# Kernel optimization log

Measured on AMD Instinct MI355X. Metric: run time of the kernel, lower is better.

Reference implementation:

```python
import jax, jax.numpy as jnp
import numpy as np

H = 1024

def _lin(x, W, b):
    # torch Linear: y = x @ W.T + b, W shape (out, in)
    return x @ W.T + b

def setup_inputs() -> dict:
    key = jax.random.key(0)
    ks = jax.random.split(key, 16)
    B, S = 128, 128
    s = 1.0 / np.sqrt(H)
    inp = {
        'facts': jax.random.normal(ks[0], (B, S, H), jnp.float32),
        'questions': jax.random.normal(ks[1], (B, 1, H), jnp.float32),
        'prevM': jax.random.normal(ks[2], (B, 1, H), jnp.float32),
        # AttentionGRUCell params
        'Wr': jax.random.normal(ks[3], (H, H), jnp.float32) * s,
        'br': jnp.zeros((H,), jnp.float32),
        'Ur': jax.random.normal(ks[4], (H, H), jnp.float32) * s,
        'bur': jnp.zeros((H,), jnp.float32),
        'W': jax.random.normal(ks[5], (H, H), jnp.float32) * s,
        'bw': jnp.zeros((H,), jnp.float32),
        'U': jax.random.normal(ks[6], (H, H), jnp.float32) * s,
        'bu': jnp.zeros((H,), jnp.float32),
        # interaction MLP
        'Wz1': jax.random.normal(ks[7], (H, 4 * H), jnp.float32) * (1.0 / np.sqrt(4 * H)),
        'bz1': jnp.zeros((H,), jnp.float32),
        'Wz2': jax.random.normal(ks[8], (1, H), jnp.float32) * s,
        'bz2': jnp.zeros((1,), jnp.float32),
        # next memory
        'Wm': jax.random.normal(ks[9], (H, 3 * H), jnp.float32) * (1.0 / np.sqrt(3 * H)),
        'bm': jnp.zeros((H,), jnp.float32),
    }
    return inp

def _forward(facts, questions, prevM, Wr, br, Ur, bur, W, bw, U, bu, Wz1, bz1, Wz2, bz2, Wm, bm):
    B, S, E = facts.shape
    q = questions  # (B,1,H) broadcasts
    m = prevM
    # gated interaction features: (B,S,4H)
    z = jnp.concatenate([facts * q, facts * m,
                         jnp.abs(facts - q), jnp.abs(facts - m)], axis=2)
    G = _lin(jnp.tanh(_lin(z, Wz1, bz1)), Wz2, bz2)  # (B,S,1)
    G = jax.nn.softmax(G[..., 0], axis=1)            # (B,S)

    # attention GRU scan over sentences
    def step(C, xs):
        fact, g = xs                                  # fact (B,H), g (B,)
        r = jax.nn.sigmoid(_lin(fact, Wr, br) + _lin(C, Ur, bur))
        h_tilda = jnp.tanh(_lin(fact, W, bw) + r * _lin(C, U, bu))
        g = g[:, None]
        C = g * h_tilda + (1.0 - g) * C
        return C, None

    C0 = jnp.zeros((B, E), facts.dtype)
    C, _ = jax.lax.scan(step, C0, (facts.transpose(1, 0, 2), G.T))

    concat = jnp.concatenate([prevM[:, 0], C, questions[:, 0]], axis=1)  # (B,3H)
    next_mem = jax.nn.relu(_lin(concat, Wm, bm))
    return next_mem[:, None, :]  # (B,1,H)

def reference(facts, questions, prevM, Wr, br, Ur, bur, W, bw, U, bu, Wz1, bz1, Wz2, bz2, Wm, bm):
    return _forward(facts, questions, prevM, Wr, br, Ur, bur, W, bw, U, bu, Wz1, bz1, Wz2, bz2, Wm, bm)
```

## Files before the change

### kernel.cpp

```cpp
#include <hip/hip_runtime.h>
#include <hip/hip_bf16.h>

typedef __attribute__((ext_vector_type(8))) short short8;
typedef __attribute__((ext_vector_type(4))) short short4v;
typedef __attribute__((ext_vector_type(4))) float floatx4;
typedef __attribute__((ext_vector_type(4))) unsigned int uint4v;

using bf16 = __hip_bfloat16;

#define DEVI __device__ __forceinline__

static constexpr size_t OFF_SCORE  = 0;
static constexpr size_t OFF_XCC    = 65536;
static constexpr size_t OFF_CPUB   = OFF_XCC + 4096;
static constexpr size_t ZERO_BYTES = OFF_CPUB + 524288;
static constexpr size_t OFF_G      = OFF_CPUB   + 1048576;
static constexpr size_t OFF_BIASR  = OFF_G      + 65536;
static constexpr size_t OFF_CFIN   = OFF_BIASR  + 4096;
static constexpr size_t OFF_CONCAT = OFF_CFIN   + 524288;
static constexpr size_t OFF_FACTS  = OFF_CONCAT + 786432;
static constexpr size_t OFF_WZ1    = OFF_FACTS  + 33554432ull;
static constexpr size_t OFF_WRW    = OFF_WZ1    + 8388608ull;
static constexpr size_t OFF_URU    = OFF_WRW    + 4194304ull;
static constexpr size_t OFF_WM     = OFF_URU    + 4194304ull;
static constexpr size_t OFF_P      = OFF_WM     + 6291456ull;

DEVI float sigm_f(float x){ return 1.f/(1.f + __expf(-x)); }
DEVI float tanh_f(float x){ float e = __expf(2.f*x); return 1.f - 2.f/(e + 1.f); }

DEVI uint4v ld_cg_u128(const uint4v* p){
  uint4v r;
  asm volatile("global_load_dwordx4 %0, %1, off sc0 sc1" : "=v"(r) : "v"(p) : "memory");
  return r;
}
DEVI uint4v ld_l2_u128(const uint4v* p){
  uint4v r;
  asm volatile("global_load_dwordx4 %0, %1, off sc0" : "=v"(r) : "v"(p) : "memory");
  return r;
}
DEVI void st_cg_u64(unsigned long long* p, unsigned long long v){
  asm volatile("global_store_dwordx2 %0, %1, off sc0 sc1" : : "v"(p), "v"(v) : "memory");
}
DEVI void st_l2_u64(unsigned long long* p, unsigned long long v){
  asm volatile("global_store_dwordx2 %0, %1, off" : : "v"(p), "v"(v) : "memory");
}
DEVI void waitcnt_vm0(){ asm volatile("s_waitcnt vmcnt(0)" ::: "memory"); }

__global__ void cast_f32_bf16(const float* __restrict__ src, bf16* __restrict__ dst, int n){
  int i = (blockIdx.x*256 + threadIdx.x)*4;
  if (i >= n) return;
  float4 v = *(const float4*)(src + i);
  union { bf16 h[4]; short4v s; } u;
  u.h[0] = __float2bfloat16(v.x); u.h[1] = __float2bfloat16(v.y);
  u.h[2] = __float2bfloat16(v.z); u.h[3] = __float2bfloat16(v.w);
  *(short4v*)(dst + i) = u.s;
}

__global__ void add_bias_k(const float* __restrict__ a, const float* __restrict__ b, float* __restrict__ o){
  int i = blockIdx.x*256 + threadIdx.x;
  if (i < 1024) o[i] = a[i] + b[i];
}

__global__ void softmax128(const float* __restrict__ score, float* __restrict__ G){
  int b = blockIdx.x, t = threadIdx.x;
  int lane = t & 63, wv = t >> 6;
  float v = score[b*128 + t];
  float mx = v;
  #pragma unroll
  for (int m = 1; m < 64; m <<= 1) mx = fmaxf(mx, __shfl_xor(mx, m));
  __shared__ float r1[2], r2[2];
  if (lane == 0) r1[wv] = mx;
  __syncthreads();
  mx = fmaxf(r1[0], r1[1]);
  float e = __expf(v - mx);
  float sm = e;
  #pragma unroll
  for (int m = 1; m < 64; m <<= 1) sm += __shfl_xor(sm, m);
  if (lane == 0) r2[wv] = sm;
  __syncthreads();
  sm = r2[0] + r2[1];
  G[b*128 + t] = e / sm;
}

__global__ void build_concat(const float* __restrict__ prevM, const float* __restrict__ Cfin,
                             const float* __restrict__ q, bf16* __restrict__ out){
  int i = (blockIdx.x*256 + threadIdx.x)*4;
  if (i >= 128*3072) return;
  int b = i / 3072, k = i % 3072;
  const float* src = (k < 1024) ? (prevM + b*1024 + k)
                   : (k < 2048) ? (Cfin + b*1024 + (k-1024))
                                : (q    + b*1024 + (k-2048));
  float4 v = *(const float4*)src;
  union { bf16 h[4]; short4v s; } u;
  u.h[0] = __float2bfloat16(v.x); u.h[1] = __float2bfloat16(v.y);
  u.h[2] = __float2bfloat16(v.z); u.h[3] = __float2bfloat16(v.w);
  *(short4v*)(out + i) = u.s;
}

__global__ __launch_bounds__(256, 2) void gate_gemm(
    const float* __restrict__ facts, const float* __restrict__ q,
    const float* __restrict__ pm, const bf16* __restrict__ Wz1b,
    const float* __restrict__ bz1, const float* __restrict__ wz2,
    float* __restrict__ score)
{
  constexpr int TS = 80;
  __shared__ bf16 As[128*TS];
  __shared__ bf16 Bs[128*TS];
  __shared__ float qs[1024];
  __shared__ float ms[1024];
  int tid = threadIdx.x;
  int b  = blockIdx.y;
  int n0 = blockIdx.x * 128;
  int w = tid >> 6, lane = tid & 63;
  int wm = w >> 1, wn = w & 1;
  int quad = lane >> 4, col = lane & 15;

  for (int i = tid; i < 1024; i += 256){ qs[i] = q[b*1024 + i]; ms[i] = pm[b*1024 + i]; }
  __syncthreads();

  floatx4 acc[4][4];
  #pragma unroll
  for (int a = 0; a < 4; ++a)
    #pragma unroll
    for (int c = 0; c < 4; ++c) acc[a][c] = (floatx4){0.f,0.f,0.f,0.f};

  for (int it = 0; it < 64; ++it){
    int k0 = it * 64;
    int qd = k0 >> 10;
    int kk0 = k0 & 1023;
    #pragma unroll
    for (int i = 0; i < 4; ++i){
      int c = tid + i*256;
      int r = c >> 3, cc = c & 7;
      int kk = kk0 + cc*8;
      const float* fp = facts + (size_t)(b*128 + r)*1024 + kk;
      float f[8], aux[8];
      *(float4*)(f)   = *(const float4*)(fp);
      *(float4*)(f+4) = *(const float4*)(fp + 4);
      const float* av = (qd == 0 || qd == 2) ? qs : ms;
      *(float4*)(aux)   = *(const float4*)(av + kk);
      *(float4*)(aux+4) = *(const float4*)(av + kk + 4);
      union { bf16 h[8]; short8 s8; } u;
      if (qd < 2){
        #pragma unroll
        for (int j = 0; j < 8; ++j) u.h[j] = __float2bfloat16(f[j]*aux[j]);
      } else {
        #pragma unroll
        for (int j = 0; j < 8; ++j) u.h[j] = __float2bfloat16(fabsf(f[j]-aux[j]));
      }
      *(short8*)&As[r*TS + cc*8] = u.s8;
    }
    #pragma unroll
    for (int i = 0; i < 4; ++i){
      int c = tid + i*256;
      int r = c >> 3, cc = c & 7;
      *(uint4v*)&Bs[r*TS + cc*8] = *(const uint4v*)(Wz1b + (size_t)(n0 + r)*4096 + k0 + cc*8);
    }
    __syncthreads();
    #pragma unroll
    for (int kt = 0; kt < 2; ++kt){
      short8 af[4], bfv[4];
      #pragma unroll
      for (int mt = 0; mt < 4; ++mt)
        af[mt] = *(const short8*)&As[(wm*64 + mt*16 + col)*TS + kt*32 + quad*8];
      #pragma unroll
      for (int nt = 0; nt < 4; ++nt)
        bfv[nt] = *(const short8*)&Bs[(wn*64 + nt*16 + col)*TS + kt*32 + quad*8];
      #pragma unroll
      for (int mt = 0; mt < 4; ++mt)
        #pragma unroll
        for (int nt = 0; nt < 4; ++nt)
          acc[mt][nt] = __builtin_amdgcn_mfma_f32_16x16x32_bf16(af[mt], bfv[nt], acc[mt][nt], 0,0,0);
    }
    __syncthreads();
  }
  #pragma unroll
  for (int mt = 0; mt < 4; ++mt){
    float part[4] = {0.f,0.f,0.f,0.f};
    #pragma unroll
    for (int nt = 0; nt < 4; ++nt){
      int n = n0 + wn*64 + nt*16 + col;
      float b1 = bz1[n], w2 = wz2[n];
      #pragma unroll
      for (int rr = 0; rr < 4; ++rr)
        part[rr] += tanh_f(acc[mt][nt][rr] + b1) * w2;
    }
    #pragma unroll
    for (int rr = 0; rr < 4; ++rr){
      float p = part[rr];
      p += __shfl_xor(p, 1); p += __shfl_xor(p, 2);
      p += __shfl_xor(p, 4); p += __shfl_xor(p, 8);
      if (col == 0)
        atomicAdd(&score[b*128 + wm*64 + mt*16 + quad*4 + rr], p);
    }
  }
}

template<int MODE>
__global__ __launch_bounds__(256, 2) void gemm_bt(
    const bf16* __restrict__ A, const bf16* __restrict__ Bm, int K,
    bf16* __restrict__ Pout, const float* __restrict__ bias, float* __restrict__ out)
{
  constexpr int TS = 80;
  __shared__ bf16 As[128*TS];
  __shared__ bf16 Bs[128*TS];
  int tid = threadIdx.x;
  int m0 = blockIdx.y * 128, n0 = blockIdx.x * 128;
  int w = tid >> 6, lane = tid & 63;
  int wm = w >> 1, wn = w & 1;
  int quad = lane >> 4, col = lane & 15;

  floatx4 acc[4][4];
  #pragma unroll
  for (int a = 0; a < 4; ++a)
    #pragma unroll
    for (int c = 0; c < 4; ++c) acc[a][c] = (floatx4){0.f,0.f,0.f,0.f};

  int nkb = K >> 6;
  for (int it = 0; it < nkb; ++it){
    int k0 = it * 64;
    #pragma unroll
    for (int i = 0; i < 4; ++i){
      int c = tid + i*256;
      int r = c >> 3, cc = c & 7;
      *(uint4v*)&As[r*TS + cc*8] = *(const uint4v*)(A  + (size_t)(m0 + r)*K + k0 + cc*8);
      *(uint4v*)&Bs[r*TS + cc*8] = *(const uint4v*)(Bm + (size_t)(n0 + r)*K + k0 + cc*8);
    }
    __syncthreads();
    #pragma unroll
    for (int kt = 0; kt < 2; ++kt){
      short8 af[4], bfv[4];
      #pragma unroll
      for (int mt = 0; mt < 4; ++mt)
        af[mt] = *(const short8*)&As[(wm*64 + mt*16 + col)*TS + kt*32 + quad*8];
      #pragma unroll
      for (int nt = 0; nt < 4; ++nt)
        bfv[nt] = *(const short8*)&Bs[(wn*64 + nt*16 + col)*TS + kt*32 + quad*8];
      #pragma unroll
      for (int mt = 0; mt < 4; ++mt)
        #pragma unroll
        for (int nt = 0; nt < 4; ++nt)
          acc[mt][nt] = __builtin_amdgcn_mfma_f32_16x16x32_bf16(af[mt], bfv[nt], acc[mt][nt], 0,0,0);
    }
    __syncthreads();
  }
  #pragma unroll
  for (int mt = 0; mt < 4; ++mt)
    #pragma unroll
    for (int nt = 0; nt < 4; ++nt)
      #pragma unroll
      for (int rr = 0; rr < 4; ++rr){
        int m = m0 + wm*64 + mt*16 + quad*4 + rr;
        int n = n0 + wn*64 + nt*16 + col;
        float v = acc[mt][nt][rr];
        if (MODE == 0){
          Pout[((size_t)(m & 127)*128 + (m >> 7))*2048 + n] = __float2bfloat16(v);
        } else {
          out[(size_t)m*1024 + n] = fmaxf(v + bias[n], 0.f);
        }
      }
}

__global__ __launch_bounds__(256, 1) void scan_kernel(
    const bf16* __restrict__ UrU, const bf16* __restrict__ P,
    const float* __restrict__ G, const float* __restrict__ bias_r,
    const float* __restrict__ bw, const float* __restrict__ bu,
    unsigned long long* __restrict__ Cpub, float* __restrict__ Cfinal,
    unsigned int* __restrict__ xcc_slots)
{
  constexpr int CS = 1040;
  __shared__ bf16 Cs[16*CS];
  __shared__ float Qex[2*16*32];
  int tid = threadIdx.x;
  int g  = blockIdx.x & 7;
  int nb = blockIdx.x >> 3;
  int b0 = g * 16, j0 = nb * 32;
  int w = tid >> 6, lane = tid & 63;
  int quad = lane >> 4, col = lane & 15;

  unsigned int my_tag = __builtin_amdgcn_s_getreg(20 | (31u << 11)) + 1u;
  bool fast;
  {
    unsigned int* xs = xcc_slots + g*32;
    if (tid == 0)
      __hip_atomic_store(&xs[nb], my_tag, __ATOMIC_RELAXED, __HIP_MEMORY_SCOPE_AGENT);
    unsigned long long bad;
    for (;;){
      unsigned int v = (lane < 32)
        ? __hip_atomic_load(&xs[lane], __ATOMIC_RELAXED, __HIP_MEMORY_SCOPE_AGENT)
        : my_tag;
      if (__ballot(v == 0u) == 0ull){ bad = __ballot(v != my_tag); break; }
      __builtin_amdgcn_s_sleep(1);
    }
    fast = (bad == 0ull);
  }

  short8 bfrag[32];
  {
    int n = ((w >> 1) << 10) + j0 + ((w & 1) << 4) + col;
    const bf16* src = UrU + (size_t)n*1024 + (quad << 3);
    #pragma unroll
    for (int kt = 0; kt < 32; ++kt) bfrag[kt] = *(const short8*)(src + kt*32);
  }

  int r  = tid >> 4;
  int jp = (tid & 15) * 2;
  float c0 = 0.f, c1 = 0.f;
  float2 brv = *(const float2*)(bias_r + j0 + jp);
  float2 bwv = *(const float2*)(bw     + j0 + jp);
  float2 buv = *(const float2*)(bu     + j0 + jp);

  for (int s = 0; s < 128; ++s){
    const bf16* Ps = P + (size_t)s*(128*2048) + (size_t)(b0 + r)*2048 + j0 + jp;
    unsigned int up1 = *(const unsigned int*)Ps;
    unsigned int up2 = *(const unsigned int*)(Ps + 1024);
    float gg = G[(b0 + r)*128 + s];

    const uint4v* Cg = (const uint4v*)
      (Cpub + (size_t)(s & 1)*65536 + (size_t)b0*512);
    uint4v vv[16];
    unsigned int expct = (unsigned int)s;
    for (;;){
      if (fast){
        #pragma unroll
        for (int i = 0; i < 16; ++i) vv[i] = ld_l2_u128(Cg + tid + i*256);
      } else {
        #pragma unroll
        for (int i = 0; i < 16; ++i) vv[i] = ld_cg_u128(Cg + tid + i*256);
      }
      waitcnt_vm0();
      unsigned int bad = 0;
      #pragma unroll
      for (int i = 0; i < 16; ++i)
        bad |= (vv[i].y ^ expct) | (vv[i].w ^ expct);
      if (__ballot(bad != 0u) == 0ull) break;
      __builtin_amdgcn_s_sleep(1);
    }
    #pragma unroll
    for (int i = 0; i < 16; ++i){
      int p = tid + i*256;
      int rr = p >> 8, pi = p & 255;
      unsigned long long wdat = (unsigned long long)vv[i].x
                              | ((unsigned long long)vv[i].z << 32);
      *(unsigned long long*)&Cs[rr*CS + pi*4] = wdat;
    }
    __syncthreads();

    floatx4 a0 = (floatx4){0.f,0.f,0.f,0.f}, a1 = (floatx4){0.f,0.f,0.f,0.f};
    {
      const bf16* Ap = Cs + col*CS + (quad << 3);
      #pragma unroll
      for (int kt = 0; kt < 16; ++kt){
        short8 a = *(const short8*)(Ap + kt*32);
        a0 = __builtin_amdgcn_mfma_f32_16x16x32_bf16(a, bfrag[kt], a0, 0,0,0);
      }
      #pragma unroll
      for (int kt = 16; kt < 32; ++kt){
        short8 a = *(const short8*)(Ap + kt*32);
        a1 = __builtin_amdgcn_mfma_f32_16x16x32_bf16(a, bfrag[kt], a1, 0,0,0);
      }
    }
    {
      int mi = w >> 1, nh = w & 1;
      #pragma unroll
      for (int rr = 0; rr < 4; ++rr)
        Qex[mi*512 + (quad*4 + rr)*32 + nh*16 + col] = a0[rr] + a1[rr];
    }
    __syncthreads();

    float p1a = __bfloat162float(*(const bf16*)&up1);
    float p1b = __bfloat162float(*((const bf16*)&up1 + 1));
    float p2a = __bfloat162float(*(const bf16*)&up2);
    float p2b = __bfloat162float(*((const bf16*)&up2 + 1));
    float2 q1 = *(const float2*)&Qex[r*32 + jp];
    float2 q2 = *(const float2*)&Qex[512 + r*32 + jp];
    float ra = sigm_f(p1a + q1.x + brv.x);
    float ha = tanh_f(p2a + bwv.x + ra*(q2.x + buv.x));
    c0 = gg*ha + (1.f - gg)*c0;
    float rb = sigm_f(p1b + q1.y + brv.y);
    float hb = tanh_f(p2b + bwv.y + rb*(q2.y + buv.y));
    c1 = gg*hb + (1.f - gg)*c1;

    if (s != 127){
      union { bf16 h[2]; unsigned int u; } pk;
      pk.h[0] = __float2bfloat16(c0);
      pk.h[1] = __float2bfloat16(c1);
      unsigned long long wd = ((unsigned long long)(unsigned int)(s + 1) << 32)
                            | (unsigned long long)pk.u;
      unsigned long long* dst = Cpub + (size_t)((s & 1) ^ 1)*65536
                              + (size_t)(b0 + r)*512 + ((j0 + jp) >> 1);
      if (fast) st_l2_u64(dst, wd); else st_cg_u64(dst, wd);
    }
  }
  *(float2*)&Cfinal[(size_t)(b0 + r)*1024 + j0 + jp] = make_float2(c0, c1);
}

extern "C" void kernel_launch(void* const* d_in, const int* in_sizes, int n_in,
                              void* d_out, int out_size, void* d_ws, size_t ws_size,
                              hipStream_t stream) {
  const float* facts     = (const float*)d_in[0];
  const float* questions = (const float*)d_in[1];
  const float* prevM     = (const float*)d_in[2];
  const float* Wr        = (const float*)d_in[3];
  const float* br        = (const float*)d_in[4];
  const float* Ur        = (const float*)d_in[5];
  const float* bur       = (const float*)d_in[6];
  const float* Wf        = (const float*)d_in[7];
  const float* bw        = (const float*)d_in[8];
  const float* U         = (const float*)d_in[9];
  const float* bu        = (const float*)d_in[10];
  const float* Wz1       = (const float*)d_in[11];
  const float* bz1       = (const float*)d_in[12];
  const float* Wz2       = (const float*)d_in[13];
  const float* Wm        = (const float*)d_in[15];
  const float* bm        = (const float*)d_in[16];
  float* out = (float*)d_out;

  char* ws = (char*)d_ws;
  float*              score   = (float*)(ws + OFF_SCORE);
  unsigned int*       xccs    = (unsigned int*)(ws + OFF_XCC);
  unsigned long long* Cpub    = (unsigned long long*)(ws + OFF_CPUB);
  float*              G       = (float*)(ws + OFF_G);
  float*              bias_r  = (float*)(ws + OFF_BIASR);
  float*              Cfin    = (float*)(ws + OFF_CFIN);
  bf16*               concat  = (bf16*)(ws + OFF_CONCAT);
  bf16*               facts_b = (bf16*)(ws + OFF_FACTS);
  bf16*               Wz1_b   = (bf16*)(ws + OFF_WZ1);
  bf16*               WrW_b   = (bf16*)(ws + OFF_WRW);
  bf16*               UrU_b   = (bf16*)(ws + OFF_URU);
  bf16*               Wm_b    = (bf16*)(ws + OFF_WM);
  bf16*               P       = (bf16*)(ws + OFF_P);

  hipMemsetAsync(ws, 0, ZERO_BYTES, stream);

  cast_f32_bf16<<<16384, 256, 0, stream>>>(facts, facts_b, 16777216);
  cast_f32_bf16<<< 4096, 256, 0, stream>>>(Wz1, Wz1_b, 4194304);
  cast_f32_bf16<<< 1024, 256, 0, stream>>>(Wr, WrW_b,           1048576);
  cast_f32_bf16<<< 1024, 256, 0, stream>>>(Wf, WrW_b + 1048576, 1048576);
  cast_f32_bf16<<< 1024, 256, 0, stream>>>(Ur, UrU_b,           1048576);
  cast_f32_bf16<<< 1024, 256, 0, stream>>>(U,  UrU_b + 1048576, 1048576);
  cast_f32_bf16<<< 3072, 256, 0, stream>>>(Wm, Wm_b, 3145728);
  add_bias_k<<<4, 256, 0, stream>>>(br, bur, bias_r);

  gate_gemm<<<dim3(8, 128), 256, 0, stream>>>(facts, questions, prevM, Wz1_b, bz1, Wz2, score);
  softmax128<<<128, 128, 0, stream>>>(score, G);

  gemm_bt<0><<<dim3(16, 128), 256, 0, stream>>>(facts_b, WrW_b, 1024, P, nullptr, nullptr);

  scan_kernel<<<256, 256, 0, stream>>>(UrU_b, P, G, bias_r, bw, bu, Cpub, Cfin, xccs);

  build_concat<<<384, 256, 0, stream>>>(prevM, Cfin, questions, concat);
  gemm_bt<1><<<dim3(8, 1), 256, 0, stream>>>(concat, Wm_b, 3072, nullptr, bm, out);
}
```

Baseline: 1.031 ms.

## Reuse facts registers across four feature quadrants and prefetch next facts tile

The Wz1 GEMM loop is restructured so each facts chunk is loaded once into registers and reused for all four interaction quadrants (f*q, f*m, |f-q|, |f-m|), instead of reloading facts from global memory per quadrant. The next facts chunk is prefetched into registers while the current one is processed, and B-tile loads are issued into registers before the LDS store. This cuts global facts traffic by about four times and overlaps load latency, at the cost of higher register pressure (two 32-float facts buffers), which could reduce occupancy.

```diff
diff --git a/kernel.cpp b/kernel.cpp
--- a/kernel.cpp
+++ b/kernel.cpp
@@ -124,56 +124,90 @@
     #pragma unroll
     for (int c = 0; c < 4; ++c) acc[a][c] = (floatx4){0.f,0.f,0.f,0.f};
 
-  for (int it = 0; it < 64; ++it){
-    int k0 = it * 64;
-    int qd = k0 >> 10;
-    int kk0 = k0 & 1023;
-    #pragma unroll
-    for (int i = 0; i < 4; ++i){
-      int c = tid + i*256;
-      int r = c >> 3, cc = c & 7;
-      int kk = kk0 + cc*8;
-      const float* fp = facts + (size_t)(b*128 + r)*1024 + kk;
-      float f[8], aux[8];
-      *(float4*)(f)   = *(const float4*)(fp);
-      *(float4*)(f+4) = *(const float4*)(fp + 4);
-      const float* av = (qd == 0 || qd == 2) ? qs : ms;
-      *(float4*)(aux)   = *(const float4*)(av + kk);
-      *(float4*)(aux+4) = *(const float4*)(av + kk + 4);
-      union { bf16 h[8]; short8 s8; } u;
-      if (qd < 2){
-        #pragma unroll
-        for (int j = 0; j < 8; ++j) u.h[j] = __float2bfloat16(f[j]*aux[j]);
-      } else {
-        #pragma unroll
-        for (int j = 0; j < 8; ++j) u.h[j] = __float2bfloat16(fabsf(f[j]-aux[j]));
-      }
-      *(short8*)&As[r*TS + cc*8] = u.s8;
-    }
-    #pragma unroll
-    for (int i = 0; i < 4; ++i){
-      int c = tid + i*256;
-      int r = c >> 3, cc = c & 7;
-      *(uint4v*)&Bs[r*TS + cc*8] = *(const uint4v*)(Wz1b + (size_t)(n0 + r)*4096 + k0 + cc*8);
-    }
-    __syncthreads();
-    #pragma unroll
-    for (int kt = 0; kt < 2; ++kt){
-      short8 af[4], bfv[4];
-      #pragma unroll
-      for (int mt = 0; mt < 4; ++mt)
-        af[mt] = *(const short8*)&As[(wm*64 + mt*16 + col)*TS + kt*32 + quad*8];
-      #pragma unroll
-      for (int nt = 0; nt < 4; ++nt)
-        bfv[nt] = *(const short8*)&Bs[(wn*64 + nt*16 + col)*TS + kt*32 + quad*8];
-      #pragma unroll
-      for (int mt = 0; mt < 4; ++mt)
+  int cc = tid & 7;
+  int r0 = tid >> 3;
+
+  float fc[4][8];
+  float fn[4][8];
+  float q8[8], m8[8];
+
+  #pragma unroll
+  for (int i = 0; i < 4; ++i){
+    const float* fp = facts + (size_t)(b*128 + r0 + i*32)*1024 + cc*8;
+    *(float4*)(fc[i])   = *(const float4*)(fp);
+    *(float4*)(fc[i]+4) = *(const float4*)(fp + 4);
+  }
+
+  for (int it = 0; it < 16; ++it){
+    int kk0 = it * 64;
+    int kk  = kk0 + cc*8;
+    *(float4*)(q8)   = *(const float4*)(qs + kk);
+    *(float4*)(q8+4) = *(const float4*)(qs + kk + 4);
+    *(float4*)(m8)   = *(const float4*)(ms + kk);
+    *(float4*)(m8+4) = *(const float4*)(ms + kk + 4);
+    if (it < 15){
+      #pragma unroll
+      for (int i = 0; i < 4; ++i){
+        const float* fp = facts + (size_t)(b*128 + r0 + i*32)*1024 + kk0 + 64 + cc*8;
+        *(float4*)(fn[i])   = *(const float4*)(fp);
+        *(float4*)(fn[i]+4) = *(const float4*)(fp + 4);
+      }
+    }
+
+    #pragma unroll
+    for (int qd = 0; qd < 4; ++qd){
+      uint4v breg[4];
+      #pragma unroll
+      for (int i = 0; i < 4; ++i)
+        breg[i] = *(const uint4v*)(Wz1b + (size_t)(n0 + r0 + i*32)*4096 + qd*1024 + kk);
+
+      #pragma unroll
+      for (int i = 0; i < 4; ++i){
+        union { bf16 h[8]; short8 s8; } u;
+        if (qd == 0){
+          #pragma unroll
+          for (int j = 0; j < 8; ++j) u.h[j] = __float2bfloat16(fc[i][j]*q8[j]);
+        } else if (qd == 1){
+          #pragma unroll
+          for (int j = 0; j < 8; ++j) u.h[j] = __float2bfloat16(fc[i][j]*m8[j]);
+        } else if (qd == 2){
+          #pragma unroll
+          for (int j = 0; j < 8; ++j) u.h[j] = __float2bfloat16(fabsf(fc[i][j]-q8[j]));
+        } else {
+          #pragma unroll
+          for (int j = 0; j < 8; ++j) u.h[j] = __float2bfloat16(fabsf(fc[i][j]-m8[j]));
+        }
+        *(short8*)&As[(r0 + i*32)*TS + cc*8] = u.s8;
+        *(uint4v*)&Bs[(r0 + i*32)*TS + cc*8] = breg[i];
+      }
+      __syncthreads();
+
+      #pragma unroll
+      for (int kt = 0; kt < 2; ++kt){
+        short8 af[4], bfv[4];
+        #pragma unroll
+        for (int mt = 0; mt < 4; ++mt)
+          af[mt] = *(const short8*)&As[(wm*64 + mt*16 + col)*TS + kt*32 + quad*8];
         #pragma unroll
         for (int nt = 0; nt < 4; ++nt)
-          acc[mt][nt] = __builtin_amdgcn_mfma_f32_16x16x32_bf16(af[mt], bfv[nt], acc[mt][nt], 0,0,0);
-    }
-    __syncthreads();
-  }
+          bfv[nt] = *(const short8*)&Bs[(wn*64 + nt*16 + col)*TS + kt*32 + quad*8];
+        #pragma unroll
+        for (int mt = 0; mt < 4; ++mt)
+          #pragma unroll
+          for (int nt = 0; nt < 4; ++nt)
+            acc[mt][nt] = __builtin_amdgcn_mfma_f32_16x16x32_bf16(af[mt], bfv[nt], acc[mt][nt], 0,0,0);
+      }
+      __syncthreads();
+    }
+
+    if (it < 15){
+      #pragma unroll
+      for (int i = 0; i < 4; ++i)
+        #pragma unroll
+        for (int j = 0; j < 8; ++j) fc[i][j] = fn[i][j];
+    }
+  }
+
   #pragma unroll
   for (int mt = 0; mt < 4; ++mt){
     float part[4] = {0.f,0.f,0.f,0.f};
```

Measured after the change: 840.5 us, median of 2. 18.5% less time.
